# Kernel tuning notes

Hardware: AMD Instinct MI355X
Metric: run time of the kernel (lower is better)

Reference implementation:

```python
import jax, jax.numpy as jnp
import numpy as np

B, L, D, H = 2, 2048, 1024, 16
HD = D // H
SCALE = HD ** -0.5


def setup_inputs() -> dict:
    key = jax.random.key(0)
    ks = jax.random.split(key, 11)
    s = D ** -0.5  # torch Linear default init scale (uniform bound)
    return {
        "q": jax.random.normal(ks[0], (B, L, D), jnp.float32),
        "k": jax.random.normal(ks[1], (B, L, D), jnp.float32),
        "v": jax.random.normal(ks[2], (B, L, D), jnp.float32),
        "Wq": jax.random.uniform(ks[3], (D, D), jnp.float32, -s, s),
        "bq": jax.random.uniform(ks[4], (D,), jnp.float32, -s, s),
        "Wk": jax.random.uniform(ks[5], (D, D), jnp.float32, -s, s),
        "bk": jax.random.uniform(ks[6], (D,), jnp.float32, -s, s),
        "Wv": jax.random.uniform(ks[7], (D, D), jnp.float32, -s, s),
        "bv": jax.random.uniform(ks[8], (D,), jnp.float32, -s, s),
        "Wo": jax.random.uniform(ks[9], (D, D), jnp.float32, -s, s),
        "bo": jax.random.uniform(ks[10], (D,), jnp.float32, -s, s),
    }


def reference(q, k, v, Wq, bq, Wk, bk, Wv, bv, Wo, bo):
    b, q_len, _ = q.shape
    # projections; weights stored as (D, D) acting on the right: x @ W + b
    qh = (q @ Wq + bq).reshape(b, q_len, H, HD).transpose(0, 2, 1, 3)  # (B,H,Q,hd)
    kh = (k @ Wk + bk).reshape(b, -1, H, HD).transpose(0, 2, 1, 3)    # (B,H,K,hd)
    vh = (v @ Wv + bv).reshape(b, -1, H, HD).transpose(0, 2, 1, 3)    # (B,H,K,hd)
    att = jnp.einsum("bhqd,bhkd->bhqk", qh * SCALE, kh)               # (B,H,Q,K)
    att = jax.nn.softmax(att, axis=-1)
    out = jnp.einsum("bhqk,bhkd->bhqd", att, vh)                      # (B,H,Q,hd)
    out = out.transpose(0, 2, 1, 3).reshape(b, q_len, D)
    return out @ Wo + bo
```

## Files before the change

### kernel.cpp

```cpp
#include <hip/hip_runtime.h>

namespace {
constexpr int kB  = 2;
constexpr int kL  = 2048;
constexpr int kD  = 1024;
constexpr int kH  = 16;
constexpr int kHD = 64;
constexpr int kM  = kB * kL;
}

typedef _Float16 f16x8 __attribute__((ext_vector_type(8)));
typedef float    f32x16 __attribute__((ext_vector_type(16)));
typedef unsigned int u32;

union Frag16 { uint4 u4; unsigned u[4]; f16x8 v; };

__device__ __forceinline__ unsigned short f2h(float f) {
    return __builtin_bit_cast(unsigned short, (_Float16)f);
}
__device__ __forceinline__ unsigned pk2(float a, float b) {
    return __builtin_bit_cast(unsigned, __builtin_amdgcn_cvt_pkrtz(a, b));
}

__device__ __forceinline__ void gload16(const void* g, void* l) {
    __builtin_amdgcn_global_load_lds(
        (const __attribute__((address_space(1))) u32*)g,
        (__attribute__((address_space(3))) u32*)(unsigned long long)(__builtin_bit_cast(unsigned long long, l)),
        16, 0, 0);
}

__global__ __launch_bounds__(256) void prep_kernel(
    const float* __restrict__ q, const float* __restrict__ k,
    const float* __restrict__ v, unsigned short* __restrict__ dstA,
    const float* __restrict__ W0, const float* __restrict__ W1,
    const float* __restrict__ W2, const float* __restrict__ W3,
    unsigned short* __restrict__ WtBase)
{
    __shared__ _Float16 T[64][68];
    const int id = blockIdx.x;
    if (id < 6144) {
        const int yy = id >> 11;
        const int xx = id & 2047;
        const float* src = yy == 0 ? q : (yy == 1 ? k : v);
        unsigned short* d = dstA + (size_t)yy * ((size_t)kM * kD);
        const size_t i = ((size_t)xx * 256 + threadIdx.x) * 8;
        const float4 f0 = *(const float4*)(src + i);
        const float4 f1 = *(const float4*)(src + i + 4);
        _Float16 h[8];
        h[0] = (_Float16)f0.x; h[1] = (_Float16)f0.y;
        h[2] = (_Float16)f0.z; h[3] = (_Float16)f0.w;
        h[4] = (_Float16)f1.x; h[5] = (_Float16)f1.y;
        h[6] = (_Float16)f1.z; h[7] = (_Float16)f1.w;
        *(uint4*)(d + i) = *(uint4*)h;
        return;
    }
    const int id2 = id - 6144;
    const int z = id2 >> 8;
    const int rem = id2 & 255;
    const int by = rem >> 4, bx = rem & 15;
    const float* W = z == 0 ? W0 : z == 1 ? W1 : z == 2 ? W2 : W3;
    unsigned short* Wt = WtBase + (size_t)z * ((size_t)kD * kD);
    const int k0 = by * 64, n0 = bx * 64;
    const int tx = threadIdx.x & 15, ty = threadIdx.x >> 4;
#pragma unroll
    for (int i = 0; i < 4; ++i) {
        const int kk = i * 16 + ty;
        const float4 w = *(const float4*)&W[(size_t)(k0 + kk) * kD + n0 + tx * 4];
        T[tx * 4 + 0][kk] = (_Float16)w.x;
        T[tx * 4 + 1][kk] = (_Float16)w.y;
        T[tx * 4 + 2][kk] = (_Float16)w.z;
        T[tx * 4 + 3][kk] = (_Float16)w.w;
    }
    __syncthreads();
#pragma unroll
    for (int i = 0; i < 4; ++i) {
        const int nn = i * 16 + ty;
        *(ushort4*)&Wt[(size_t)(n0 + nn) * kD + k0 + tx * 4] = *(ushort4*)&T[nn][tx * 4];
    }
}

__global__ __launch_bounds__(256) void gemm_qkv_kernel(
    const unsigned short* __restrict__ A, const unsigned short* __restrict__ Wt,
    const float* __restrict__ bq, const float* __restrict__ bk,
    const float* __restrict__ bv, unsigned short* __restrict__ Qh,
    unsigned short* __restrict__ Kh, unsigned short* __restrict__ Vt)
{
    __shared__ unsigned short Als[2][128 * 64];
    __shared__ unsigned short Bls[2][128 * 64];

    const int tid = threadIdx.x;
    const int lane = tid & 63;
    const int wid = tid >> 6;
    const int l31 = lane & 31;
    const int hi = lane >> 5;
    const int by = blockIdx.x & 31;
    const int bxp = blockIdx.x >> 5;
    const int proj = bxp >> 3;
    const int bx = bxp & 7;
    const int row0 = by * 128;
    const int col0 = bx * 128;
    const int wr = wid >> 1, wc = wid & 1;

    const int rl = lane >> 3;
    const int sl = lane & 7;
    const int ssrc = (sl ^ rl) * 8;

    const unsigned short* Aproj = A + (size_t)proj * ((size_t)kM * kD);
    const unsigned short* Wproj = Wt + (size_t)proj * ((size_t)kD * kD);
    const unsigned short* Abase = Aproj + (size_t)(row0 + wid * 32 + rl) * kD + ssrc;
    const unsigned short* Bbase = Wproj + (size_t)(col0 + wid * 32 + rl) * kD + ssrc;

    f32x16 acc00{}, acc01{}, acc10{}, acc11{};

    auto stage = [&](int kt, int buf) {
#pragma unroll
        for (int i = 0; i < 4; ++i) {
            gload16(Abase + (size_t)(i * 8) * kD + kt * 64,
                    &Als[buf][(wid * 32 + i * 8) * 64]);
        }
#pragma unroll
        for (int i = 0; i < 4; ++i) {
            gload16(Bbase + (size_t)(i * 8) * kD + kt * 64,
                    &Bls[buf][(wid * 32 + i * 8) * 64]);
        }
    };

    const int ra0 = wr * 64 + l31;
    const int cb0 = wc * 64 + l31;

    stage(0, 0);
    int cur = 0;
    for (int kt = 0; kt < kD / 64; ++kt) {
        __syncthreads();
        if (kt + 1 < kD / 64) stage(kt + 1, cur ^ 1);
#pragma unroll
        for (int ks = 0; ks < 4; ++ks) {
            const int slot = (ks << 1) | hi;
            Frag16 a0, a1, b0, b1;
            a0.u4 = *(const uint4*)&Als[cur][ra0 * 64 + ((slot ^ (ra0 & 7)) << 3)];
            a1.u4 = *(const uint4*)&Als[cur][(ra0 + 32) * 64 + ((slot ^ ((ra0 + 32) & 7)) << 3)];
            b0.u4 = *(const uint4*)&Bls[cur][cb0 * 64 + ((slot ^ (cb0 & 7)) << 3)];
            b1.u4 = *(const uint4*)&Bls[cur][(cb0 + 32) * 64 + ((slot ^ ((cb0 + 32) & 7)) << 3)];
            acc00 = __builtin_amdgcn_mfma_f32_32x32x16_f16(a0.v, b0.v, acc00, 0, 0, 0);
            acc01 = __builtin_amdgcn_mfma_f32_32x32x16_f16(a0.v, b1.v, acc01, 0, 0, 0);
            acc10 = __builtin_amdgcn_mfma_f32_32x32x16_f16(a1.v, b0.v, acc10, 0, 0, 0);
            acc11 = __builtin_amdgcn_mfma_f32_32x32x16_f16(a1.v, b1.v, acc11, 0, 0, 0);
        }
        cur ^= 1;
    }

    const float* bias = proj == 0 ? bq : (proj == 1 ? bk : bv);
    const float bias0 = bias[col0 + wc * 64 + l31];
    const float bias1 = bias[col0 + wc * 64 + 32 + l31];
    const float oscale = proj == 0 ? (0.125f * 1.44269504089f) : 1.0f;

    const f32x16* accs[2][2] = {{&acc00, &acc01}, {&acc10, &acc11}};
#pragma unroll
    for (int rt = 0; rt < 2; ++rt) {
#pragma unroll
        for (int ct = 0; ct < 2; ++ct) {
            const f32x16& acv = *accs[rt][ct];
            const float bb = ct ? bias1 : bias0;
            const int c = col0 + wc * 64 + ct * 32 + l31;
            if (proj == 2) {
#pragma unroll
                for (int qd = 0; qd < 4; ++qd) {
                    const int r = row0 + wr * 64 + rt * 32 + 8 * qd + 4 * hi;
                    const int b_ = r >> 11;
                    int l_ = r & (kL - 1);
                    l_ ^= ((((l_ >> 2) ^ (l_ >> 3)) & 1) ? 12 : 0);
                    ushort4 w;
                    w.x = f2h(acv[4 * qd + 0] + bb);
                    w.y = f2h(acv[4 * qd + 1] + bb);
                    w.z = f2h(acv[4 * qd + 2] + bb);
                    w.w = f2h(acv[4 * qd + 3] + bb);
                    *(ushort4*)&Vt[((size_t)(b_ * kH + (c >> 6)) * kHD + (c & 63)) * kL + l_] = w;
                }
            } else {
                unsigned short* C = proj == 0 ? Qh : Kh;
#pragma unroll
                for (int reg = 0; reg < 16; ++reg) {
                    const int r = row0 + wr * 64 + rt * 32 + (reg & 3) + 8 * (reg >> 2) + 4 * hi;
                    const int b_ = r >> 11, l_ = r & (kL - 1);
                    C[((size_t)(b_ * kH + (c >> 6)) * kL + l_) * kHD + (c & 63)] =
                        f2h((acv[reg] + bb) * oscale);
                }
            }
        }
    }
}

__global__ __launch_bounds__(256) void gemm_o_kernel(
    const unsigned short* __restrict__ A, const unsigned short* __restrict__ Wt,
    const float* __restrict__ bias, float* __restrict__ C)
{
    __shared__ unsigned short Als[2][128 * 64];
    __shared__ unsigned short Bls[2][64 * 64];

    const int tid = threadIdx.x;
    const int lane = tid & 63;
    const int wid = tid >> 6;
    const int l31 = lane & 31;
    const int hi = lane >> 5;
    const int by = blockIdx.x & 31;
    const int bx = blockIdx.x >> 5;
    const int row0 = by * 128;
    const int wr = wid >> 1, wc = wid & 1;

    const int rl = lane >> 3;
    const int sl = lane & 7;
    const int ssrc = (sl ^ rl) * 8;

    const unsigned short* Abase = A + (size_t)(row0 + wid * 32 + rl) * kD + ssrc;
    const unsigned short* Bbase = Wt + (size_t)(bx * 64 + wid * 16 + rl) * kD + ssrc;

    f32x16 acc0{}, acc1{};

    auto stage = [&](int kt, int buf) {
#pragma unroll
        for (int i = 0; i < 4; ++i)
            gload16(Abase + (size_t)(i * 8) * kD + kt * 64,
                    &Als[buf][(wid * 32 + i * 8) * 64]);
        gload16(Bbase + kt * 64,                   &Bls[buf][(wid * 16) * 64]);
        gload16(Bbase + (size_t)8 * kD + kt * 64,  &Bls[buf][(wid * 16 + 8) * 64]);
    };

    const int ra0 = wr * 64 + l31;
    const int cb0 = wc * 32 + l31;

    stage(0, 0);
    int cur = 0;
    for (int kt = 0; kt < kD / 64; ++kt) {
        __syncthreads();
        if (kt + 1 < kD / 64) stage(kt + 1, cur ^ 1);
#pragma unroll
        for (int ks = 0; ks < 4; ++ks) {
            const int slot = (ks << 1) | hi;
            Frag16 a0, a1, b0;
            a0.u4 = *(const uint4*)&Als[cur][ra0 * 64 + ((slot ^ (ra0 & 7)) << 3)];
            a1.u4 = *(const uint4*)&Als[cur][(ra0 + 32) * 64 + ((slot ^ ((ra0 + 32) & 7)) << 3)];
            b0.u4 = *(const uint4*)&Bls[cur][cb0 * 64 + ((slot ^ (cb0 & 7)) << 3)];
            acc0 = __builtin_amdgcn_mfma_f32_32x32x16_f16(a0.v, b0.v, acc0, 0, 0, 0);
            acc1 = __builtin_amdgcn_mfma_f32_32x32x16_f16(a1.v, b0.v, acc1, 0, 0, 0);
        }
        cur ^= 1;
    }

    const int c = (bx << 6) + wc * 32 + l31;
    const float bb = bias[c];
    const f32x16* accs[2] = {&acc0, &acc1};
#pragma unroll
    for (int rt = 0; rt < 2; ++rt) {
        const f32x16& acv = *accs[rt];
#pragma unroll
        for (int reg = 0; reg < 16; ++reg) {
            const int r = row0 + wr * 64 + rt * 32 + (reg & 3) + 8 * (reg >> 2) + 4 * hi;
            C[(size_t)r * kD + c] = acv[reg] + bb;
        }
    }
}

__global__ __launch_bounds__(512) void attn_mfma_kernel(
    const unsigned short* __restrict__ Qh, const unsigned short* __restrict__ Kh,
    const unsigned short* __restrict__ Vt, unsigned short* __restrict__ Opart,
    float2* __restrict__ Stat)
{
    __shared__ unsigned short Kls[4][64 * 64];
    __shared__ unsigned short Vls[4][64 * 64];

    const int lane = threadIdx.x & 63;
    const int wid  = threadIdx.x >> 6;
    const int l31  = lane & 31;
    const int hi   = lane >> 5;

    const int id = blockIdx.x;
    const int j  = id >> 3;
    const int bh = (id & 7) * 4 + (j >> 4);
    const int qt = j & 7;
    const int ks = (j >> 3) & 1;
    const int q = qt * 256 + wid * 32 + l31;

    const size_t qkBase = (size_t)bh * kL * kHD;
    const unsigned short* Qp = Qh + qkBase + (size_t)q * kHD + hi * 8;
    Frag16 qf[4];
#pragma unroll
    for (int d = 0; d < 4; ++d) qf[d].u4 = *(const uint4*)(Qp + d * 16);

    const int srow = wid * 8 + (lane >> 3);
    const int soff = (((lane & 7) ^ (srow & 7)) << 3);
    const unsigned short* Kg = Kh + qkBase + (size_t)srow * kHD + soff;
    const unsigned short* Vg = Vt + (size_t)bh * kHD * kL + (size_t)srow * kL + soff;

    auto stage = [&](int kt, int buf) {
        gload16(Kg + (size_t)(kt * 64) * kHD, &Kls[buf][(wid * 8) * 64]);
        gload16(Vg + kt * 64,                 &Vls[buf][(wid * 8) * 64]);
    };

    f32x16 o0{}, o1{};
    float lsum = 0.f;
    const int rA = l31, rB = l31 + 32;

    const int kt0 = ks * 16;
    stage(kt0 + 0, 0);
    stage(kt0 + 1, 1);

    for (int rt = 0; rt < 8; ++rt) {
        const int t0 = 2 * rt;
        asm volatile("s_waitcnt vmcnt(0)" ::: "memory");
        __builtin_amdgcn_s_barrier();
        if (t0 + 3 < 16) {
            stage(kt0 + t0 + 2, (t0 + 2) & 3);
            stage(kt0 + t0 + 3, (t0 + 3) & 3);
        }
        const int bA = t0 & 3, bB = (t0 + 1) & 3;

        f32x16 c0{}, c1{}, c2{}, c3{};
        __builtin_amdgcn_s_setprio(1);
#pragma unroll
        for (int d = 0; d < 4; ++d) {
            const int s = (d << 1) | hi;
            Frag16 ka0, ka1, kb0, kb1;
            ka0.u4 = *(const uint4*)&Kls[bA][rA * 64 + ((s ^ (rA & 7)) << 3)];
            ka1.u4 = *(const uint4*)&Kls[bA][rB * 64 + ((s ^ (rB & 7)) << 3)];
            kb0.u4 = *(const uint4*)&Kls[bB][rA * 64 + ((s ^ (rA & 7)) << 3)];
            kb1.u4 = *(const uint4*)&Kls[bB][rB * 64 + ((s ^ (rB & 7)) << 3)];
            c0 = __builtin_amdgcn_mfma_f32_32x32x16_f16(ka0.v, qf[d].v, c0, 0, 0, 0);
            c1 = __builtin_amdgcn_mfma_f32_32x32x16_f16(ka1.v, qf[d].v, c1, 0, 0, 0);
            c2 = __builtin_amdgcn_mfma_f32_32x32x16_f16(kb0.v, qf[d].v, c2, 0, 0, 0);
            c3 = __builtin_amdgcn_mfma_f32_32x32x16_f16(kb1.v, qf[d].v, c3, 0, 0, 0);
        }
        __builtin_amdgcn_s_setprio(0);

        float rs = 0.f;
        Frag16 pfA[4], pfB[4];
#pragma unroll
        for (int i = 0; i < 8; ++i) {
            const float e0 = __builtin_amdgcn_exp2f(c0[2 * i]);
            const float e1 = __builtin_amdgcn_exp2f(c0[2 * i + 1]);
            const float e2 = __builtin_amdgcn_exp2f(c1[2 * i]);
            const float e3 = __builtin_amdgcn_exp2f(c1[2 * i + 1]);
            const float e4 = __builtin_amdgcn_exp2f(c2[2 * i]);
            const float e5 = __builtin_amdgcn_exp2f(c2[2 * i + 1]);
            const float e6 = __builtin_amdgcn_exp2f(c3[2 * i]);
            const float e7 = __builtin_amdgcn_exp2f(c3[2 * i + 1]);
            pfA[i >> 2].u[i & 3]       = pk2(e0, e1);
            pfA[2 + (i >> 2)].u[i & 3] = pk2(e2, e3);
            pfB[i >> 2].u[i & 3]       = pk2(e4, e5);
            pfB[2 + (i >> 2)].u[i & 3] = pk2(e6, e7);
            rs += ((e0 + e1) + (e2 + e3)) + ((e4 + e5) + (e6 + e7));
        }
        rs += __shfl_xor(rs, 32);
        lsum += rs;

        __builtin_amdgcn_s_setprio(1);
#pragma unroll
        for (int ksl = 0; ksl < 4; ++ksl) {
            const int s = (ksl << 1) | hi;
            Frag16 v0, v1;
            v0.u4 = *(const uint4*)&Vls[bA][rA * 64 + ((s ^ (rA & 7)) << 3)];
            v1.u4 = *(const uint4*)&Vls[bA][rB * 64 + ((s ^ (rB & 7)) << 3)];
            o0 = __builtin_amdgcn_mfma_f32_32x32x16_f16(v0.v, pfA[ksl].v, o0, 0, 0, 0);
            o1 = __builtin_amdgcn_mfma_f32_32x32x16_f16(v1.v, pfA[ksl].v, o1, 0, 0, 0);
        }
#pragma unroll
        for (int ksl = 0; ksl < 4; ++ksl) {
            const int s = (ksl << 1) | hi;
            Frag16 v0, v1;
            v0.u4 = *(const uint4*)&Vls[bB][rA * 64 + ((s ^ (rA & 7)) << 3)];
            v1.u4 = *(const uint4*)&Vls[bB][rB * 64 + ((s ^ (rB & 7)) << 3)];
            o0 = __builtin_amdgcn_mfma_f32_32x32x16_f16(v0.v, pfB[ksl].v, o0, 0, 0, 0);
            o1 = __builtin_amdgcn_mfma_f32_32x32x16_f16(v1.v, pfB[ksl].v, o1, 0, 0, 0);
        }
        __builtin_amdgcn_s_setprio(0);
    }

    const size_t prow = (size_t)ks * (32 * kL) + (size_t)bh * kL + q;
    const float inv = 1.f / lsum;
    unsigned short* pp = Opart + prow * kHD;
#pragma unroll
    for (int g = 0; g < 4; ++g) {
        const int d = g * 8 + hi * 4;
        uint2 w0, w1;
        w0.x = pk2(o0[4 * g + 0] * inv, o0[4 * g + 1] * inv);
        w0.y = pk2(o0[4 * g + 2] * inv, o0[4 * g + 3] * inv);
        w1.x = pk2(o1[4 * g + 0] * inv, o1[4 * g + 1] * inv);
        w1.y = pk2(o1[4 * g + 2] * inv, o1[4 * g + 3] * inv);
        *(uint2*)(pp + d) = w0;
        *(uint2*)(pp + 32 + d) = w1;
    }
    if (hi == 0) Stat[prow] = make_float2(0.f, lsum);
}

__global__ __launch_bounds__(256) void merge_kernel(
    const unsigned short* __restrict__ Opart, const float2* __restrict__ Stat,
    unsigned short* __restrict__ O16)
{
    const int g = blockIdx.x * 256 + threadIdx.x;
    const int row = g >> 3;
    const int d0 = (g & 7) * 8;
    const int bh = row >> 11, q = row & (kL - 1);
    const float2 sa = Stat[row];
    const float2 sb = Stat[32 * kL + row];
    float wa = sa.y;
    float wb = sb.y;
    const float inv = 1.f / (wa + wb);
    wa *= inv; wb *= inv;

    const unsigned short* pa = Opart + (size_t)row * kHD + d0;
    const unsigned short* pb = pa + (size_t)32 * kL * kHD;
    uint4 ua = *(const uint4*)pa;
    uint4 ub = *(const uint4*)pb;
    _Float16 ha[8], hb[8];
    *(uint4*)ha = ua;
    *(uint4*)hb = ub;
    unsigned out[4];
#pragma unroll
    for (int i = 0; i < 4; ++i) {
        const float v0 = wa * (float)ha[2 * i]     + wb * (float)hb[2 * i];
        const float v1 = wa * (float)ha[2 * i + 1] + wb * (float)hb[2 * i + 1];
        out[i] = pk2(v0, v1);
    }
    const int b_ = bh >> 4, h_ = bh & 15;
    *(uint4*)&O16[((size_t)(b_ * kL + q)) * kD + h_ * kHD + d0] = *(uint4*)out;
}

extern "C" void kernel_launch(void* const* d_in, const int* in_sizes, int n_in,
                              void* d_out, int out_size, void* d_ws, size_t ws_size,
                              hipStream_t stream)
{
    const float* q  = (const float*)d_in[0];
    const float* k  = (const float*)d_in[1];
    const float* v  = (const float*)d_in[2];
    const float* Wq = (const float*)d_in[3];
    const float* bq = (const float*)d_in[4];
    const float* Wk = (const float*)d_in[5];
    const float* bk = (const float*)d_in[6];
    const float* Wv = (const float*)d_in[7];
    const float* bv = (const float*)d_in[8];
    const float* Wo = (const float*)d_in[9];
    const float* bo = (const float*)d_in[10];
    float* out = (float*)d_out;

    const size_t MD = (size_t)kM * kD;
    const size_t DD = (size_t)kD * kD;
    unsigned short* A16 = (unsigned short*)d_ws;
    unsigned short* Wt16 = A16 + 3 * MD;
    unsigned short* Qh16 = Wt16 + 4 * DD;
    unsigned short* Kh16 = Qh16 + MD;
    unsigned short* Vt16 = Kh16 + MD;
    unsigned short* O16   = A16;
    unsigned short* Opart = A16 + MD;
    float2*         Stat  = (float2*)Wt16;

    const dim3 blk(256);

    hipLaunchKernelGGL(prep_kernel, dim3(7168), blk, 0, stream,
                       q, k, v, A16, Wq, Wk, Wv, Wo, Wt16);

    hipLaunchKernelGGL(gemm_qkv_kernel, dim3(32 * 24), blk, 0, stream,
                       A16, Wt16, bq, bk, bv, Qh16, Kh16, Vt16);

    hipLaunchKernelGGL(attn_mfma_kernel, dim3(512), dim3(512), 0, stream,
                       Qh16, Kh16, Vt16, Opart, Stat);
    hipLaunchKernelGGL(merge_kernel, dim3(2048), blk, 0, stream,
                       Opart, Stat, O16);

    hipLaunchKernelGGL(gemm_o_kernel, dim3(32 * 16), blk, 0, stream,
                       O16, Wt16 + 3 * DD, bo, out);
}
```

Baseline: 123.0 us.

## Split attention into four KV chunks with smaller blocks and four-way merge

The attention kernel now uses 256-thread blocks covering 128 queries, and splits the key range into four chunks of 512 instead of two chunks of 1024, launching 2048 blocks instead of 512. Each iteration processes one 64-key tile with double buffering, prefetching the next tile and waiting only on the older loads. The merge kernel combines four partial outputs weighted by their row sums. Workspace buffers are rearranged so the extra partials fit. The goal is more blocks for better occupancy and load balance across CUs, at the cost of more partial-output traffic and a heavier merge.

```diff
diff --git a/kernel.cpp b/kernel.cpp
--- a/kernel.cpp
+++ b/kernel.cpp
@@ -260,13 +260,13 @@
     }
 }
 
-__global__ __launch_bounds__(512) void attn_mfma_kernel(
+__global__ __launch_bounds__(256) void attn_mfma_kernel(
     const unsigned short* __restrict__ Qh, const unsigned short* __restrict__ Kh,
-    const unsigned short* __restrict__ Vt, unsigned short* __restrict__ Opart,
-    float2* __restrict__ Stat)
-{
-    __shared__ unsigned short Kls[4][64 * 64];
-    __shared__ unsigned short Vls[4][64 * 64];
+    const unsigned short* __restrict__ Vt, unsigned short* __restrict__ OpA,
+    unsigned short* __restrict__ OpB, float2* __restrict__ Stat)
+{
+    __shared__ unsigned short Kls[2][64 * 64];
+    __shared__ unsigned short Vls[2][64 * 64];
 
     const int lane = threadIdx.x & 63;
     const int wid  = threadIdx.x >> 6;
@@ -275,10 +275,11 @@
 
     const int id = blockIdx.x;
     const int j  = id >> 3;
-    const int bh = (id & 7) * 4 + (j >> 4);
-    const int qt = j & 7;
-    const int ks = (j >> 3) & 1;
-    const int q = qt * 256 + wid * 32 + l31;
+    const int bh = (id & 7) * 4 + (j >> 6);
+    const int rem = j & 63;
+    const int qt = rem & 15;
+    const int ks = rem >> 4;
+    const int q = qt * 128 + wid * 32 + l31;
 
     const size_t qkBase = (size_t)bh * kL * kHD;
     const unsigned short* Qp = Qh + qkBase + (size_t)q * kHD + hi * 8;
@@ -286,97 +287,75 @@
 #pragma unroll
     for (int d = 0; d < 4; ++d) qf[d].u4 = *(const uint4*)(Qp + d * 16);
 
-    const int srow = wid * 8 + (lane >> 3);
+    const int srow = wid * 16 + (lane >> 3);
     const int soff = (((lane & 7) ^ (srow & 7)) << 3);
     const unsigned short* Kg = Kh + qkBase + (size_t)srow * kHD + soff;
     const unsigned short* Vg = Vt + (size_t)bh * kHD * kL + (size_t)srow * kL + soff;
 
     auto stage = [&](int kt, int buf) {
-        gload16(Kg + (size_t)(kt * 64) * kHD, &Kls[buf][(wid * 8) * 64]);
-        gload16(Vg + kt * 64,                 &Vls[buf][(wid * 8) * 64]);
+        gload16(Kg + (size_t)(kt * 64) * kHD,     &Kls[buf][(wid * 16) * 64]);
+        gload16(Kg + (size_t)(kt * 64 + 8) * kHD, &Kls[buf][(wid * 16 + 8) * 64]);
+        gload16(Vg + kt * 64,                     &Vls[buf][(wid * 16) * 64]);
+        gload16(Vg + kt * 64 + (size_t)8 * kL,    &Vls[buf][(wid * 16 + 8) * 64]);
     };
 
     f32x16 o0{}, o1{};
     float lsum = 0.f;
     const int rA = l31, rB = l31 + 32;
 
-    const int kt0 = ks * 16;
+    const int kt0 = ks * 8;
     stage(kt0 + 0, 0);
-    stage(kt0 + 1, 1);
-
-    for (int rt = 0; rt < 8; ++rt) {
-        const int t0 = 2 * rt;
-        asm volatile("s_waitcnt vmcnt(0)" ::: "memory");
+
+    for (int t = 0; t < 8; ++t) {
+        if (t < 7) asm volatile("s_waitcnt vmcnt(4)" ::: "memory");
+        else       asm volatile("s_waitcnt vmcnt(0)" ::: "memory");
         __builtin_amdgcn_s_barrier();
-        if (t0 + 3 < 16) {
-            stage(kt0 + t0 + 2, (t0 + 2) & 3);
-            stage(kt0 + t0 + 3, (t0 + 3) & 3);
-        }
-        const int bA = t0 & 3, bB = (t0 + 1) & 3;
-
-        f32x16 c0{}, c1{}, c2{}, c3{};
+        if (t + 1 < 8) stage(kt0 + t + 1, (t + 1) & 1);
+        const int cur = t & 1;
+
+        f32x16 c0{}, c1{};
         __builtin_amdgcn_s_setprio(1);
 #pragma unroll
         for (int d = 0; d < 4; ++d) {
             const int s = (d << 1) | hi;
-            Frag16 ka0, ka1, kb0, kb1;
-            ka0.u4 = *(const uint4*)&Kls[bA][rA * 64 + ((s ^ (rA & 7)) << 3)];
-            ka1.u4 = *(const uint4*)&Kls[bA][rB * 64 + ((s ^ (rB & 7)) << 3)];
-            kb0.u4 = *(const uint4*)&Kls[bB][rA * 64 + ((s ^ (rA & 7)) << 3)];
-            kb1.u4 = *(const uint4*)&Kls[bB][rB * 64 + ((s ^ (rB & 7)) << 3)];
+            Frag16 ka0, ka1;
+            ka0.u4 = *(const uint4*)&Kls[cur][rA * 64 + ((s ^ (rA & 7)) << 3)];
+            ka1.u4 = *(const uint4*)&Kls[cur][rB * 64 + ((s ^ (rB & 7)) << 3)];
             c0 = __builtin_amdgcn_mfma_f32_32x32x16_f16(ka0.v, qf[d].v, c0, 0, 0, 0);
             c1 = __builtin_amdgcn_mfma_f32_32x32x16_f16(ka1.v, qf[d].v, c1, 0, 0, 0);
-            c2 = __builtin_amdgcn_mfma_f32_32x32x16_f16(kb0.v, qf[d].v, c2, 0, 0, 0);
-            c3 = __builtin_amdgcn_mfma_f32_32x32x16_f16(kb1.v, qf[d].v, c3, 0, 0, 0);
         }
         __builtin_amdgcn_s_setprio(0);
 
-        float rs = 0.f;
-        Frag16 pfA[4], pfB[4];
+        Frag16 pf[4];
 #pragma unroll
         for (int i = 0; i < 8; ++i) {
             const float e0 = __builtin_amdgcn_exp2f(c0[2 * i]);
             const float e1 = __builtin_amdgcn_exp2f(c0[2 * i + 1]);
             const float e2 = __builtin_amdgcn_exp2f(c1[2 * i]);
             const float e3 = __builtin_amdgcn_exp2f(c1[2 * i + 1]);
-            const float e4 = __builtin_amdgcn_exp2f(c2[2 * i]);
-            const float e5 = __builtin_amdgcn_exp2f(c2[2 * i + 1]);
-            const float e6 = __builtin_amdgcn_exp2f(c3[2 * i]);
-            const float e7 = __builtin_amdgcn_exp2f(c3[2 * i + 1]);
-            pfA[i >> 2].u[i & 3]       = pk2(e0, e1);
-            pfA[2 + (i >> 2)].u[i & 3] = pk2(e2, e3);
-            pfB[i >> 2].u[i & 3]       = pk2(e4, e5);
-            pfB[2 + (i >> 2)].u[i & 3] = pk2(e6, e7);
-            rs += ((e0 + e1) + (e2 + e3)) + ((e4 + e5) + (e6 + e7));
-        }
-        rs += __shfl_xor(rs, 32);
-        lsum += rs;
+            pf[i >> 2].u[i & 3]       = pk2(e0, e1);
+            pf[2 + (i >> 2)].u[i & 3] = pk2(e2, e3);
+            lsum += (e0 + e1) + (e2 + e3);
+        }
 
         __builtin_amdgcn_s_setprio(1);
 #pragma unroll
         for (int ksl = 0; ksl < 4; ++ksl) {
             const int s = (ksl << 1) | hi;
             Frag16 v0, v1;
-            v0.u4 = *(const uint4*)&Vls[bA][rA * 64 + ((s ^ (rA & 7)) << 3)];
-            v1.u4 = *(const uint4*)&Vls[bA][rB * 64 + ((s ^ (rB & 7)) << 3)];
-            o0 = __builtin_amdgcn_mfma_f32_32x32x16_f16(v0.v, pfA[ksl].v, o0, 0, 0, 0);
-            o1 = __builtin_amdgcn_mfma_f32_32x32x16_f16(v1.v, pfA[ksl].v, o1, 0, 0, 0);
-        }
-#pragma unroll
-        for (int ksl = 0; ksl < 4; ++ksl) {
-            const int s = (ksl << 1) | hi;
-            Frag16 v0, v1;
-            v0.u4 = *(const uint4*)&Vls[bB][rA * 64 + ((s ^ (rA & 7)) << 3)];
-            v1.u4 = *(const uint4*)&Vls[bB][rB * 64 + ((s ^ (rB & 7)) << 3)];
-            o0 = __builtin_amdgcn_mfma_f32_32x32x16_f16(v0.v, pfB[ksl].v, o0, 0, 0, 0);
-            o1 = __builtin_amdgcn_mfma_f32_32x32x16_f16(v1.v, pfB[ksl].v, o1, 0, 0, 0);
+            v0.u4 = *(const uint4*)&Vls[cur][rA * 64 + ((s ^ (rA & 7)) << 3)];
+            v1.u4 = *(const uint4*)&Vls[cur][rB * 64 + ((s ^ (rB & 7)) << 3)];
+            o0 = __builtin_amdgcn_mfma_f32_32x32x16_f16(v0.v, pf[ksl].v, o0, 0, 0, 0);
+            o1 = __builtin_amdgcn_mfma_f32_32x32x16_f16(v1.v, pf[ksl].v, o1, 0, 0, 0);
         }
         __builtin_amdgcn_s_setprio(0);
     }
 
-    const size_t prow = (size_t)ks * (32 * kL) + (size_t)bh * kL + q;
+    lsum += __shfl_xor(lsum, 32);
     const float inv = 1.f / lsum;
-    unsigned short* pp = Opart + prow * kHD;
+    const size_t MDv = (size_t)32 * kL * kHD;
+    unsigned short* base = (ks < 3) ? (OpA + (size_t)ks * MDv) : OpB;
+    unsigned short* pp = base + ((size_t)bh * kL + q) * kHD;
 #pragma unroll
     for (int g = 0; g < 4; ++g) {
         const int d = g * 8 + hi * 4;
@@ -388,36 +367,41 @@
         *(uint2*)(pp + d) = w0;
         *(uint2*)(pp + 32 + d) = w1;
     }
-    if (hi == 0) Stat[prow] = make_float2(0.f, lsum);
+    if (hi == 0) Stat[(size_t)ks * (32 * kL) + (size_t)bh * kL + q]
+                     = make_float2(0.f, lsum);
 }
 
 __global__ __launch_bounds__(256) void merge_kernel(
-    const unsigned short* __restrict__ Opart, const float2* __restrict__ Stat,
-    unsigned short* __restrict__ O16)
+    const unsigned short* __restrict__ OpA, const unsigned short* __restrict__ OpB,
+    const float2* __restrict__ Stat, unsigned short* __restrict__ O16)
 {
     const int g = blockIdx.x * 256 + threadIdx.x;
     const int row = g >> 3;
     const int d0 = (g & 7) * 8;
     const int bh = row >> 11, q = row & (kL - 1);
-    const float2 sa = Stat[row];
-    const float2 sb = Stat[32 * kL + row];
-    float wa = sa.y;
-    float wb = sb.y;
-    const float inv = 1.f / (wa + wb);
-    wa *= inv; wb *= inv;
-
-    const unsigned short* pa = Opart + (size_t)row * kHD + d0;
-    const unsigned short* pb = pa + (size_t)32 * kL * kHD;
-    uint4 ua = *(const uint4*)pa;
-    uint4 ub = *(const uint4*)pb;
-    _Float16 ha[8], hb[8];
-    *(uint4*)ha = ua;
-    *(uint4*)hb = ub;
+    const float2 s0 = Stat[row];
+    const float2 s1 = Stat[32 * kL + row];
+    const float2 s2 = Stat[2 * 32 * kL + row];
+    const float2 s3 = Stat[3 * 32 * kL + row];
+    const float inv = 1.f / (s0.y + s1.y + s2.y + s3.y);
+    const float w0s = s0.y * inv, w1s = s1.y * inv;
+    const float w2s = s2.y * inv, w3s = s3.y * inv;
+
+    const size_t MDv = (size_t)32 * kL * kHD;
+    const size_t off = (size_t)row * kHD + d0;
+    uint4 u0 = *(const uint4*)(OpA + off);
+    uint4 u1 = *(const uint4*)(OpA + MDv + off);
+    uint4 u2 = *(const uint4*)(OpA + 2 * MDv + off);
+    uint4 u3 = *(const uint4*)(OpB + off);
+    _Float16 h0[8], h1[8], h2[8], h3[8];
+    *(uint4*)h0 = u0; *(uint4*)h1 = u1; *(uint4*)h2 = u2; *(uint4*)h3 = u3;
     unsigned out[4];
 #pragma unroll
     for (int i = 0; i < 4; ++i) {
-        const float v0 = wa * (float)ha[2 * i]     + wb * (float)hb[2 * i];
-        const float v1 = wa * (float)ha[2 * i + 1] + wb * (float)hb[2 * i + 1];
+        const float v0 = w0s * (float)h0[2 * i] + w1s * (float)h1[2 * i]
+                       + w2s * (float)h2[2 * i] + w3s * (float)h3[2 * i];
+        const float v1 = w0s * (float)h0[2 * i + 1] + w1s * (float)h1[2 * i + 1]
+                       + w2s * (float)h2[2 * i + 1] + w3s * (float)h3[2 * i + 1];
         out[i] = pk2(v0, v1);
     }
     const int b_ = bh >> 4, h_ = bh & 15;
@@ -448,9 +432,10 @@
     unsigned short* Qh16 = Wt16 + 4 * DD;
     unsigned short* Kh16 = Qh16 + MD;
     unsigned short* Vt16 = Kh16 + MD;
-    unsigned short* O16   = A16;
-    unsigned short* Opart = A16 + MD;
-    float2*         Stat  = (float2*)Wt16;
+    unsigned short* OpB  = Vt16 + MD;
+    unsigned short* OpA  = A16;
+    unsigned short* O16  = Vt16;
+    float2*         Stat = (float2*)Wt16;
 
     const dim3 blk(256);
 
@@ -460,10 +445,10 @@
     hipLaunchKernelGGL(gemm_qkv_kernel, dim3(32 * 24), blk, 0, stream,
                        A16, Wt16, bq, bk, bv, Qh16, Kh16, Vt16);
 
-    hipLaunchKernelGGL(attn_mfma_kernel, dim3(512), dim3(512), 0, stream,
-                       Qh16, Kh16, Vt16, Opart, Stat);
+    hipLaunchKernelGGL(attn_mfma_kernel, dim3(2048), blk, 0, stream,
+                       Qh16, Kh16, Vt16, OpA, OpB, Stat);
     hipLaunchKernelGGL(merge_kernel, dim3(2048), blk, 0, stream,
-                       Opart, Stat, O16);
+                       OpA, OpB, Stat, O16);
 
     hipLaunchKernelGGL(gemm_o_kernel, dim3(32 * 16), blk, 0, stream,
                        O16, Wt16 + 3 * DD, bo, out);
```

Result: slower. 126.3 us (+2.7%).
